# Performance work log

Hardware: AMD Instinct MI355X
Metric: run time of the kernel (lower is better)

## Reference

```python
import jax, jax.numpy as jnp
import numpy as np

# Rs_hidden = [(16,0),(16,1)] -> 16 scalar irreps (dim 1) then 16 vector irreps (dim 3)
B, N, M = 4, 80, 16
CH = M + 3 * M  # 64 channels
RADII = jnp.linspace(0.0, 1.0, 3)
GAMMA = 1.0 / (0.5 ** 2)  # gaussian rbf width = radii spacing
EPS = 1e-6

_lc = np.zeros((3, 3, 3), np.float32)
for i, j, k in [(0, 1, 2), (1, 2, 0), (2, 0, 1)]:
    _lc[i, j, k] = 1.0
    _lc[i, k, j] = -1.0
LC = jnp.asarray(_lc)  # Levi-Civita


def _si(t, w0, w1):
    """SelfInteraction: per-l mixing of multiplicities. t: [B, mi0 + 3*mi1, ...]."""
    mi0, mi1 = w0.shape[1], w1.shape[1]
    s = t[:, :mi0]
    v = t[:, mi0:].reshape(t.shape[0], mi1, 3, *t.shape[2:])
    os = jnp.einsum('om,nm...->no...', w0, s)
    ov = jnp.einsum('om,nmi...->noi...', w1, v)
    ov = ov.reshape(ov.shape[0], ov.shape[1] * 3, *ov.shape[3:])
    return jnp.concatenate([os, ov], axis=1)


def _norm_act(t, act):
    """NormActivation: scalar irreps -> act(x); vector irreps -> x * act(||x||)/||x||. Channel axis 1."""
    s = act(t[:, :M])
    v = t[:, M:].reshape(t.shape[0], M, 3, *t.shape[2:])
    n = jnp.sqrt(jnp.sum(v * v, axis=2, keepdims=True) + EPS)
    v = (v * act(n) / n).reshape(t.shape[0], 3 * M, *t.shape[2:])
    return jnp.concatenate([s, v], axis=1)


def _gate_mul(gate, target):
    """gate_normwise_multiply: multiply each irrep block of target by the L2 norm of the
    corresponding gate block (norm over the irrep components, channel axis 1)."""
    gs = jnp.abs(gate[:, :M])
    gv = gate[:, M:].reshape(gate.shape[0], M, 3, *gate.shape[2:])
    gn = jnp.sqrt(jnp.sum(gv * gv, axis=2) + EPS)
    factor = jnp.concatenate([gs, jnp.repeat(gn, 3, axis=1)], axis=1)
    return factor * target


def _interleave(a_t, b_t):
    """Interleave per-(m,l) blocks: [a_l0, b_l0, a_l1, b_l1] -> Rs_hidden_double layout."""
    return jnp.concatenate([a_t[:, :M], b_t[:, :M], a_t[:, M:], b_t[:, M:]], axis=1)


def _kernel(h_nei_diff, w_k00, w_k10, w_k01, w_k11):
    """SE3 point kernel for l in {0,1}, J<=2. Returns K[n,b,a,d,c] with d,c in irrep layout."""
    rad = jnp.sqrt(jnp.sum(h_nei_diff ** 2, axis=-1) + EPS)      # [B,N,N]
    nh = h_nei_diff / rad[..., None]                              # unit vectors
    rbf = jnp.exp(-GAMMA * (rad[..., None] - RADII) ** 2)        # [B,N,N,3]
    K00 = jnp.einsum('uvk,...k->...uv', w_k00, rbf)              # [B,N,N,M,M]
    K10 = jnp.einsum('uvk,...k,...i->...uiv', w_k10, rbf, nh).reshape(B, N, N, 3 * M, M)
    K01 = jnp.einsum('uvk,...k,...j->...uvj', w_k01, rbf, nh).reshape(B, N, N, M, 3 * M)
    RJ = jnp.einsum('juvk,...k->j...uv', w_k11, rbf)             # [3,B,N,N,M,M]
    eye = jnp.eye(3, dtype=rbf.dtype)
    cross = jnp.einsum('ijk,...k->...ij', LC, nh)                # J=1 basis
    outer = nh[..., :, None] * nh[..., None, :] - eye / 3.0      # J=2 basis
    base = (RJ[0][..., None, None] * eye
            + RJ[1][..., None, None] * cross[..., None, None, :, :]
            + RJ[2][..., None, None] * outer[..., None, None, :, :])  # [B,N,N,u,v,i,j]
    K11 = jnp.transpose(base, (0, 1, 2, 3, 5, 4, 6)).reshape(B, N, N, 3 * M, 3 * M)
    top = jnp.concatenate([K00, K01], axis=-1)
    bot = jnp.concatenate([K10, K11], axis=-1)
    return jnp.concatenate([top, bot], axis=-2)                  # [B,N,N,CH,CH]


def setup_inputs() -> dict:
    key = jax.random.key(0)
    ks = jax.random.split(key, 16)
    sc = 0.1
    d = {
        'x': jax.random.normal(ks[0], (B, CH, N), jnp.float32),
        'h_nei': jax.random.normal(ks[1], (B, CH, N), jnp.float32),
        'h_nei_diff': jax.random.normal(ks[2], (B, N, N, 3), jnp.float32),
        'mask': jax.random.uniform(ks[3], (B, N, N), jnp.float32),
        'w_k00': jax.random.normal(ks[4], (M, M, 3), jnp.float32) * sc,
        'w_k10': jax.random.normal(ks[5], (M, M, 3), jnp.float32) * sc,
        'w_k01': jax.random.normal(ks[6], (M, M, 3), jnp.float32) * sc,
        'w_k11': jax.random.normal(ks[7], (3, M, M, 3), jnp.float32) * sc,
        'si_z_w0': jax.random.normal(ks[8], (M, 2 * M), jnp.float32) * sc,
        'si_z_w1': jax.random.normal(ks[9], (M, 2 * M), jnp.float32) * sc,
        'si_r1_w0': jax.random.normal(ks[10], (M, M), jnp.float32) * sc,
        'si_r1_w1': jax.random.normal(ks[11], (M, M), jnp.float32) * sc,
        'si_r2_w0': jax.random.normal(ks[12], (M, M), jnp.float32) * sc,
        'si_r2_w1': jax.random.normal(ks[13], (M, M), jnp.float32) * sc,
        'si_ph_w0': jax.random.normal(ks[14], (M, 2 * M), jnp.float32) * sc,
        'si_ph_w1': jax.random.normal(ks[15], (M, 2 * M), jnp.float32) * sc,
    }
    return d


def reference(x, h_nei, h_nei_diff, mask, w_k00, w_k10, w_k01, w_k11,
              si_z_w0, si_z_w1, si_r1_w0, si_r1_w1, si_r2_w0, si_r2_w1,
              si_ph_w0, si_ph_w1):
    Kmat = _kernel(h_nei_diff, w_k00, w_k10, w_k01, w_k11)
    # masked neighbor conv: h_conv[n,d,b,a] = sum_c h_nei[n,c,a] K[n,b,a,d,c] mask[n,b,a]
    h_conv = jnp.einsum('nca,nbadc,nba->ndba', h_nei, Kmat, mask)
    sum_h = h_conv.sum(axis=-1)                                   # [B,CH,N]
    z = _norm_act(_si(_interleave(x, sum_h), si_z_w0, si_z_w1), jax.nn.sigmoid)
    r1 = _si(x, si_r1_w0, si_r1_w1)                               # [B,CH,N]
    r2 = _si(h_conv.reshape(B, CH, N * N), si_r2_w0, si_r2_w1).reshape(B, CH, N, N)
    r = _norm_act(r1[:, :, None, :] + r2, jax.nn.sigmoid)         # [B,CH,N,N]
    gated = _gate_mul(r, h_conv)
    sum_g = gated.sum(axis=-1)                                    # [B,CH,N]
    pre_h = _norm_act(_si(_interleave(x, sum_g), si_ph_w0, si_ph_w1), jnp.tanh)
    new_h = sum_h + _gate_mul(z, pre_h + sum_h)
    return new_h
```

## Files before the change

### kernel.cpp

```cpp
#include <hip/hip_runtime.h>
#include <math.h>

#define Bq 4
#define Nq 80
#define Mq 16
#define CHq 64
#define GAMMAq 4.0f
#define EPSq 1e-6f
#define NCOMP 46

__global__ __launch_bounds__(256) void se3_precomp(
    const float* __restrict__ h_nei,
    const float* __restrict__ x,
    const float* __restrict__ w00,
    const float* __restrict__ w10,
    const float* __restrict__ w01,
    const float* __restrict__ w11,
    const float* __restrict__ wr10,
    const float* __restrict__ wr11,
    float* __restrict__ pc)
{
    int t  = blockIdx.x * blockDim.x + threadIdx.x;
    int u  = t & 15;
    int na = t >> 4;
    int n  = na / Nq, a = na % Nq;

    const float* hb = h_nei + (size_t)n * CHq * Nq + a;
    float s[16];
    float V[16][3];
#pragma unroll
    for (int v = 0; v < 16; ++v) s[v] = hb[v * Nq];
#pragma unroll
    for (int v = 0; v < 16; ++v)
#pragma unroll
        for (int j = 0; j < 3; ++j) V[v][j] = hb[(16 + v * 3 + j) * Nq];

    float outc[NCOMP];

#pragma unroll
    for (int k = 0; k < 3; ++k) {
        float a00 = 0.f, a10 = 0.f;
#pragma unroll
        for (int v = 0; v < 16; ++v) {
            a00 += w00[(u * 16 + v) * 3 + k] * s[v];
            a10 += w10[(u * 16 + v) * 3 + k] * s[v];
        }
        outc[k]     = a00;
        outc[3 + k] = a10;
    }

#pragma unroll
    for (int k = 0; k < 3; ++k) {
        float c[3]  = {0.f, 0.f, 0.f};
        float p0[3] = {0.f, 0.f, 0.f};
        float p1[3] = {0.f, 0.f, 0.f};
        float p2[3] = {0.f, 0.f, 0.f};
#pragma unroll
        for (int v = 0; v < 16; ++v) {
            float w01v = w01[(u * 16 + v) * 3 + k];
            float w110 = w11[((0 * 16 + u) * 16 + v) * 3 + k];
            float w111 = w11[((1 * 16 + u) * 16 + v) * 3 + k];
            float w112 = w11[((2 * 16 + u) * 16 + v) * 3 + k];
#pragma unroll
            for (int j = 0; j < 3; ++j) {
                c[j]  += w01v * V[v][j];
                p0[j] += w110 * V[v][j];
                p1[j] += w111 * V[v][j];
                p2[j] += w112 * V[v][j];
            }
        }
#pragma unroll
        for (int j = 0; j < 3; ++j) {
            outc[6  + k * 3 + j] = c[j];
            outc[15 + k * 3 + j] = p0[j];
            outc[24 + k * 3 + j] = p1[j];
            outc[33 + k * 3 + j] = p2[j];
        }
    }

    const float* xb = x + (size_t)n * CHq * Nq + a;
    float r1s = 0.f, r1v[3] = {0.f, 0.f, 0.f};
#pragma unroll
    for (int v = 0; v < 16; ++v) {
        r1s += wr10[u * 16 + v] * xb[v * Nq];
        float wv = wr11[u * 16 + v];
#pragma unroll
        for (int j = 0; j < 3; ++j) r1v[j] += wv * xb[(16 + v * 3 + j) * Nq];
    }
    outc[42] = r1s;
#pragma unroll
    for (int j = 0; j < 3; ++j) outc[43 + j] = r1v[j];

    float* p = pc + (size_t)na * NCOMP * 16;
#pragma unroll
    for (int c = 0; c < NCOMP; ++c) p[c * 16 + u] = outc[c];
}

__global__ __launch_bounds__(256) void se3_main(
    const float* __restrict__ x,
    const float* __restrict__ hdiff,
    const float* __restrict__ mask,
    const float* __restrict__ wr20,
    const float* __restrict__ wr21,
    const float* __restrict__ wz0,
    const float* __restrict__ wz1,
    const float* __restrict__ wp0,
    const float* __restrict__ wp1,
    const float* __restrict__ pc,
    float* __restrict__ out)
{
    const int nb    = blockIdx.x;
    const int n     = nb / Nq;
    const int bnode = nb % Nq;
    const int tid   = threadIdx.x;
    const int g     = tid >> 4;
    const int u     = tid & 15;

    __shared__ float hcsh[16][65];
    __shared__ float redH[16][68];
    __shared__ float redG[16][68];
    __shared__ float sumH[64], sumG[64];
    __shared__ float wr2s[2][256];

    wr2s[0][tid] = wr20[tid];
    wr2s[1][tid] = wr21[tid];
    __syncthreads();

    float shs = 0.f, shv0 = 0.f, shv1 = 0.f, shv2 = 0.f;
    float sgs = 0.f, sgv0 = 0.f, sgv1 = 0.f, sgv2 = 0.f;

    for (int abase = 0; abase < Nq; abase += 16) {
        const int a = abase + g;

        const float* dp = hdiff + ((size_t)(n * Nq + bnode) * Nq + a) * 3;
        const float d0 = dp[0], d1 = dp[1], d2 = dp[2];
        const float m  = mask[(size_t)(n * Nq + bnode) * Nq + a];

        const float rad = sqrtf(d0 * d0 + d1 * d1 + d2 * d2 + EPSq);
        const float inv = 1.0f / rad;
        const float nh0 = d0 * inv, nh1 = d1 * inv, nh2 = d2 * inv;
        float rb[3];
        rb[0] = expf(-GAMMAq * rad * rad);
        { float t1 = rad - 0.5f; rb[1] = expf(-GAMMAq * t1 * t1); }
        { float t2 = rad - 1.0f; rb[2] = expf(-GAMMAq * t2 * t2); }

        const float* p = pc + (size_t)(n * Nq + a) * NCOMP * 16 + u;

        float as_ = 0.f, a10 = 0.f;
        float c01[3] = {0.f, 0.f, 0.f};
        float p0[3]  = {0.f, 0.f, 0.f};
        float p1[3]  = {0.f, 0.f, 0.f};
        float p2[3]  = {0.f, 0.f, 0.f};
#pragma unroll
        for (int k = 0; k < 3; ++k) {
            const float r = rb[k];
            as_ += r * p[(0 + k) * 16];
            a10 += r * p[(3 + k) * 16];
#pragma unroll
            for (int j = 0; j < 3; ++j) {
                c01[j] += r * p[(6  + k * 3 + j) * 16];
                p0[j]  += r * p[(15 + k * 3 + j) * 16];
                p1[j]  += r * p[(24 + k * 3 + j) * 16];
                p2[j]  += r * p[(33 + k * 3 + j) * 16];
            }
        }

        const float hcs = m * (as_ + c01[0] * nh0 + c01[1] * nh1 + c01[2] * nh2);
        const float cr0 = p1[1] * nh2 - p1[2] * nh1;
        const float cr1 = p1[2] * nh0 - p1[0] * nh2;
        const float cr2 = p1[0] * nh1 - p1[1] * nh0;
        const float pd  = p2[0] * nh0 + p2[1] * nh1 + p2[2] * nh2;
        const float third = 1.0f / 3.0f;
        const float hv0 = m * (nh0 * a10 + p0[0] + cr0 + nh0 * pd - p2[0] * third);
        const float hv1 = m * (nh1 * a10 + p0[1] + cr1 + nh1 * pd - p2[1] * third);
        const float hv2 = m * (nh2 * a10 + p0[2] + cr2 + nh2 * pd - p2[2] * third);

        hcsh[g][u]              = hcs;
        hcsh[g][16 + u * 3 + 0] = hv0;
        hcsh[g][16 + u * 3 + 1] = hv1;
        hcsh[g][16 + u * 3 + 2] = hv2;
        __syncthreads();

        float r2s = 0.f, r2v0 = 0.f, r2v1 = 0.f, r2v2 = 0.f;
#pragma unroll
        for (int v = 0; v < 16; ++v) {
            r2s += wr2s[0][u * 16 + v] * hcsh[g][v];
            const float w = wr2s[1][u * 16 + v];
            r2v0 += w * hcsh[g][16 + v * 3 + 0];
            r2v1 += w * hcsh[g][16 + v * 3 + 1];
            r2v2 += w * hcsh[g][16 + v * 3 + 2];
        }

        const float r1s  = p[42 * 16];
        const float r1v0 = p[43 * 16], r1v1 = p[44 * 16], r1v2 = p[45 * 16];
        const float rs   = 1.0f / (1.0f + expf(-(r1s + r2s)));
        const float wv0 = r1v0 + r2v0, wv1 = r1v1 + r2v1, wv2 = r1v2 + r2v2;
        const float nn  = sqrtf(wv0 * wv0 + wv1 * wv1 + wv2 * wv2 + EPSq);
        const float sc  = (1.0f / (1.0f + expf(-nn))) / nn;
        const float rv0 = wv0 * sc, rv1 = wv1 * sc, rv2 = wv2 * sc;
        const float fs  = fabsf(rs);
        const float fv  = sqrtf(rv0 * rv0 + rv1 * rv1 + rv2 * rv2 + EPSq);

        shs += hcs;        shv0 += hv0;      shv1 += hv1;      shv2 += hv2;
        sgs += fs * hcs;   sgv0 += fv * hv0; sgv1 += fv * hv1; sgv2 += fv * hv2;
        __syncthreads();
    }

    redH[g][u]              = shs;
    redH[g][16 + u * 3 + 0] = shv0;
    redH[g][16 + u * 3 + 1] = shv1;
    redH[g][16 + u * 3 + 2] = shv2;
    redG[g][u]              = sgs;
    redG[g][16 + u * 3 + 0] = sgv0;
    redG[g][16 + u * 3 + 1] = sgv1;
    redG[g][16 + u * 3 + 2] = sgv2;
    __syncthreads();

    if (tid < 64) {
        float sh = 0.f, sg = 0.f;
#pragma unroll
        for (int gg = 0; gg < 16; ++gg) { sh += redH[gg][tid]; sg += redG[gg][tid]; }
        sumH[tid] = sh;
        sumG[tid] = sg;
    }
    __syncthreads();

    if (tid < 16) {
        const float* xb = x + (size_t)n * CHq * Nq + bnode;

        float zs_in = 0.f, ps_in = 0.f;
        float zv[3] = {0.f, 0.f, 0.f};
        float pv[3] = {0.f, 0.f, 0.f};
#pragma unroll
        for (int mm = 0; mm < 32; ++mm) {
            float Sh, Sg;
            if (mm < 16) { const float xv = xb[mm * Nq]; Sh = xv; Sg = xv; }
            else         { Sh = sumH[mm - 16]; Sg = sumG[mm - 16]; }
            zs_in += wz0[tid * 32 + mm] * Sh;
            ps_in += wp0[tid * 32 + mm] * Sg;
            const float wz = wz1[tid * 32 + mm];
            const float wp = wp1[tid * 32 + mm];
#pragma unroll
            for (int j = 0; j < 3; ++j) {
                float Vh, Vg;
                if (mm < 16) { const float xv = xb[(16 + mm * 3 + j) * Nq]; Vh = xv; Vg = xv; }
                else { Vh = sumH[16 + (mm - 16) * 3 + j]; Vg = sumG[16 + (mm - 16) * 3 + j]; }
                zv[j] += wz * Vh;
                pv[j] += wp * Vg;
            }
        }

        const float zs  = 1.0f / (1.0f + expf(-zs_in));
        const float zn  = sqrtf(zv[0] * zv[0] + zv[1] * zv[1] + zv[2] * zv[2] + EPSq);
        const float zsc = (1.0f / (1.0f + expf(-zn))) / zn;
        const float zv0 = zv[0] * zsc, zv1 = zv[1] * zsc, zv2 = zv[2] * zsc;
        const float phs = tanhf(ps_in);
        const float pn  = sqrtf(pv[0] * pv[0] + pv[1] * pv[1] + pv[2] * pv[2] + EPSq);
        const float psc = tanhf(pn) / pn;
        const float pv0 = pv[0] * psc, pv1 = pv[1] * psc, pv2 = pv[2] * psc;
        const float gfs = fabsf(zs);
        const float gfv = sqrtf(zv0 * zv0 + zv1 * zv1 + zv2 * zv2 + EPSq);

        float* ob = out + (size_t)n * CHq * Nq + bnode;
        const float sh_s = sumH[tid];
        ob[tid * Nq] = sh_s + gfs * (phs + sh_s);
        const float shv_0 = sumH[16 + tid * 3 + 0];
        const float shv_1 = sumH[16 + tid * 3 + 1];
        const float shv_2 = sumH[16 + tid * 3 + 2];
        ob[(16 + tid * 3 + 0) * Nq] = shv_0 + gfv * (pv0 + shv_0);
        ob[(16 + tid * 3 + 1) * Nq] = shv_1 + gfv * (pv1 + shv_1);
        ob[(16 + tid * 3 + 2) * Nq] = shv_2 + gfv * (pv2 + shv_2);
    }
}

extern "C" void kernel_launch(void* const* d_in, const int* in_sizes, int n_in,
                              void* d_out, int out_size, void* d_ws, size_t ws_size,
                              hipStream_t stream) {
    const float* x      = (const float*)d_in[0];
    const float* h_nei  = (const float*)d_in[1];
    const float* hdiff  = (const float*)d_in[2];
    const float* mask   = (const float*)d_in[3];
    const float* w00    = (const float*)d_in[4];
    const float* w10    = (const float*)d_in[5];
    const float* w01    = (const float*)d_in[6];
    const float* w11    = (const float*)d_in[7];
    const float* wz0    = (const float*)d_in[8];
    const float* wz1    = (const float*)d_in[9];
    const float* wr10   = (const float*)d_in[10];
    const float* wr11   = (const float*)d_in[11];
    const float* wr20   = (const float*)d_in[12];
    const float* wr21   = (const float*)d_in[13];
    const float* wp0    = (const float*)d_in[14];
    const float* wp1    = (const float*)d_in[15];
    float* out = (float*)d_out;
    float* pc  = (float*)d_ws;

    se3_precomp<<<(Bq * Nq * 16 + 255) / 256, 256, 0, stream>>>(
        h_nei, x, w00, w10, w01, w11, wr10, wr11, pc);
    se3_main<<<Bq * Nq, 256, 0, stream>>>(
        x, hdiff, mask, wr20, wr21, wz0, wz1, wp0, wp1, pc, out);
}
```

Before: 29.87 us.

## Split precompute across radial basis index and widen main kernel to 512 threads

The precompute kernel now assigns one thread per (node, k, u) instead of per (node, u), giving three times as many threads, each writing directly to the workspace without a large register array. The main kernel doubles the block to 512 threads so each block covers 32 neighbours per iteration: three padded iterations over 96 slots, with out-of-range slots clamped and masked to zero. The aim is more parallelism and fewer serial loop trips per block. The cost is redundant h_nei loads per thread, some wasted padded work, and larger shared memory per block.

```diff
diff --git a/kernel.cpp b/kernel.cpp
--- a/kernel.cpp
+++ b/kernel.cpp
@@ -20,10 +20,12 @@
     const float* __restrict__ wr11,
     float* __restrict__ pc)
 {
-    int t  = blockIdx.x * blockDim.x + threadIdx.x;
-    int u  = t & 15;
-    int na = t >> 4;
-    int n  = na / Nq, a = na % Nq;
+    const int t   = blockIdx.x * blockDim.x + threadIdx.x;
+    const int na  = t / 48;
+    const int rem = t - na * 48;
+    const int k   = rem >> 4;
+    const int u   = rem & 15;
+    const int n   = na / Nq, a = na - (na / Nq) * Nq;
 
     const float* hb = h_nei + (size_t)n * CHq * Nq + a;
     float s[16];
@@ -35,32 +37,30 @@
 #pragma unroll
         for (int j = 0; j < 3; ++j) V[v][j] = hb[(16 + v * 3 + j) * Nq];
 
-    float outc[NCOMP];
-
-#pragma unroll
-    for (int k = 0; k < 3; ++k) {
+    float* pcb = pc + (size_t)na * NCOMP * 16 + u;
+
+    {
         float a00 = 0.f, a10 = 0.f;
 #pragma unroll
         for (int v = 0; v < 16; ++v) {
             a00 += w00[(u * 16 + v) * 3 + k] * s[v];
             a10 += w10[(u * 16 + v) * 3 + k] * s[v];
         }
-        outc[k]     = a00;
-        outc[3 + k] = a10;
-    }
-
-#pragma unroll
-    for (int k = 0; k < 3; ++k) {
+        pcb[(0 + k) * 16] = a00;
+        pcb[(3 + k) * 16] = a10;
+    }
+
+    {
         float c[3]  = {0.f, 0.f, 0.f};
         float p0[3] = {0.f, 0.f, 0.f};
         float p1[3] = {0.f, 0.f, 0.f};
         float p2[3] = {0.f, 0.f, 0.f};
 #pragma unroll
         for (int v = 0; v < 16; ++v) {
-            float w01v = w01[(u * 16 + v) * 3 + k];
-            float w110 = w11[((0 * 16 + u) * 16 + v) * 3 + k];
-            float w111 = w11[((1 * 16 + u) * 16 + v) * 3 + k];
-            float w112 = w11[((2 * 16 + u) * 16 + v) * 3 + k];
+            const float w01v = w01[(u * 16 + v) * 3 + k];
+            const float w110 = w11[((0 * 16 + u) * 16 + v) * 3 + k];
+            const float w111 = w11[((1 * 16 + u) * 16 + v) * 3 + k];
+            const float w112 = w11[((2 * 16 + u) * 16 + v) * 3 + k];
 #pragma unroll
             for (int j = 0; j < 3; ++j) {
                 c[j]  += w01v * V[v][j];
@@ -71,32 +71,30 @@
         }
 #pragma unroll
         for (int j = 0; j < 3; ++j) {
-            outc[6  + k * 3 + j] = c[j];
-            outc[15 + k * 3 + j] = p0[j];
-            outc[24 + k * 3 + j] = p1[j];
-            outc[33 + k * 3 + j] = p2[j];
-        }
-    }
-
-    const float* xb = x + (size_t)n * CHq * Nq + a;
-    float r1s = 0.f, r1v[3] = {0.f, 0.f, 0.f};
-#pragma unroll
-    for (int v = 0; v < 16; ++v) {
-        r1s += wr10[u * 16 + v] * xb[v * Nq];
-        float wv = wr11[u * 16 + v];
-#pragma unroll
-        for (int j = 0; j < 3; ++j) r1v[j] += wv * xb[(16 + v * 3 + j) * Nq];
-    }
-    outc[42] = r1s;
-#pragma unroll
-    for (int j = 0; j < 3; ++j) outc[43 + j] = r1v[j];
-
-    float* p = pc + (size_t)na * NCOMP * 16;
-#pragma unroll
-    for (int c = 0; c < NCOMP; ++c) p[c * 16 + u] = outc[c];
+            pcb[(6  + k * 3 + j) * 16] = c[j];
+            pcb[(15 + k * 3 + j) * 16] = p0[j];
+            pcb[(24 + k * 3 + j) * 16] = p1[j];
+            pcb[(33 + k * 3 + j) * 16] = p2[j];
+        }
+    }
+
+    if (k == 0) {
+        const float* xb = x + (size_t)n * CHq * Nq + a;
+        float r1s = 0.f, r1v[3] = {0.f, 0.f, 0.f};
+#pragma unroll
+        for (int v = 0; v < 16; ++v) {
+            r1s += wr10[u * 16 + v] * xb[v * Nq];
+            const float wv = wr11[u * 16 + v];
+#pragma unroll
+            for (int j = 0; j < 3; ++j) r1v[j] += wv * xb[(16 + v * 3 + j) * Nq];
+        }
+        pcb[42 * 16] = r1s;
+#pragma unroll
+        for (int j = 0; j < 3; ++j) pcb[(43 + j) * 16] = r1v[j];
+    }
 }
 
-__global__ __launch_bounds__(256) void se3_main(
+__global__ __launch_bounds__(512) void se3_main(
     const float* __restrict__ x,
     const float* __restrict__ hdiff,
     const float* __restrict__ mask,
@@ -111,30 +109,34 @@
 {
     const int nb    = blockIdx.x;
     const int n     = nb / Nq;
-    const int bnode = nb % Nq;
+    const int bnode = nb - n * Nq;
     const int tid   = threadIdx.x;
     const int g     = tid >> 4;
     const int u     = tid & 15;
 
-    __shared__ float hcsh[16][65];
-    __shared__ float redH[16][68];
-    __shared__ float redG[16][68];
+    __shared__ float hcsh[32][65];
+    __shared__ float redH[32][68];
+    __shared__ float redG[32][68];
     __shared__ float sumH[64], sumG[64];
     __shared__ float wr2s[2][256];
 
-    wr2s[0][tid] = wr20[tid];
-    wr2s[1][tid] = wr21[tid];
+    if (tid < 256) {
+        wr2s[0][tid] = wr20[tid];
+        wr2s[1][tid] = wr21[tid];
+    }
     __syncthreads();
 
     float shs = 0.f, shv0 = 0.f, shv1 = 0.f, shv2 = 0.f;
     float sgs = 0.f, sgv0 = 0.f, sgv1 = 0.f, sgv2 = 0.f;
 
-    for (int abase = 0; abase < Nq; abase += 16) {
-        const int a = abase + g;
-
-        const float* dp = hdiff + ((size_t)(n * Nq + bnode) * Nq + a) * 3;
+    for (int abase = 0; abase < 96; abase += 32) {
+        const int a      = abase + g;
+        const bool valid = (a < Nq);
+        const int  ac    = valid ? a : (Nq - 1);
+
+        const float* dp = hdiff + ((size_t)(n * Nq + bnode) * Nq + ac) * 3;
         const float d0 = dp[0], d1 = dp[1], d2 = dp[2];
-        const float m  = mask[(size_t)(n * Nq + bnode) * Nq + a];
+        const float m  = valid ? mask[(size_t)(n * Nq + bnode) * Nq + ac] : 0.0f;
 
         const float rad = sqrtf(d0 * d0 + d1 * d1 + d2 * d2 + EPSq);
         const float inv = 1.0f / rad;
@@ -144,7 +146,7 @@
         { float t1 = rad - 0.5f; rb[1] = expf(-GAMMAq * t1 * t1); }
         { float t2 = rad - 1.0f; rb[2] = expf(-GAMMAq * t2 * t2); }
 
-        const float* p = pc + (size_t)(n * Nq + a) * NCOMP * 16 + u;
+        const float* p = pc + (size_t)(n * Nq + ac) * NCOMP * 16 + u;
 
         float as_ = 0.f, a10 = 0.f;
         float c01[3] = {0.f, 0.f, 0.f};
@@ -219,7 +221,7 @@
     if (tid < 64) {
         float sh = 0.f, sg = 0.f;
 #pragma unroll
-        for (int gg = 0; gg < 16; ++gg) { sh += redH[gg][tid]; sg += redG[gg][tid]; }
+        for (int gg = 0; gg < 32; ++gg) { sh += redH[gg][tid]; sg += redG[gg][tid]; }
         sumH[tid] = sh;
         sumG[tid] = sg;
     }
@@ -295,8 +297,8 @@
     float* out = (float*)d_out;
     float* pc  = (float*)d_ws;
 
-    se3_precomp<<<(Bq * Nq * 16 + 255) / 256, 256, 0, stream>>>(
+    se3_precomp<<<60, 256, 0, stream>>>(
         h_nei, x, w00, w10, w01, w11, wr10, wr11, pc);
-    se3_main<<<Bq * Nq, 256, 0, stream>>>(
+    se3_main<<<Bq * Nq, 512, 0, stream>>>(
         x, hdiff, mask, wr20, wr21, wz0, wz1, wp0, wp1, pc, out);
 }
```

Result: slower. 41.18 us (+37.9%).
